# Optimization experiments

Hardware: AMD Instinct MI355X
Metric: run time of the kernel (lower is better)

The kernel has to match this reference:

```python
import jax, jax.numpy as jnp
import numpy as np

D = 13        # input_dim == cell hidden dim == attention dim
NCLASSES = 8

def conv2d(x, w):
    # x: [B,C,H,W], w: [O,I,kh,kw], SAME padding, stride 1
    return jax.lax.conv_general_dilated(x, w, (1, 1), 'SAME',
        dimension_numbers=('NCHW', 'OIHW', 'NCHW'))

def setup_inputs() -> dict:
    key = jax.random.key(0)
    ks = jax.random.split(key, 11)
    b, t, h, w = 32, 24, 32, 32
    s = 0.1
    return {
        'x1':      jax.random.normal(ks[0], (b, t, D, h, w), jnp.float32),
        'W_gates': jax.random.normal(ks[1], (4 * D, 2 * D, 3, 3), jnp.float32) * s,  # ConvLSTM gate conv on [x;h]
        'W_q':     jax.random.normal(ks[2], (D, D), jnp.float32) * s,   # SAM 1x1 convs (stored as matrices)
        'W_kh':    jax.random.normal(ks[3], (D, D), jnp.float32) * s,
        'W_vh':    jax.random.normal(ks[4], (D, D), jnp.float32) * s,
        'W_km':    jax.random.normal(ks[5], (D, D), jnp.float32) * s,
        'W_vm':    jax.random.normal(ks[6], (D, D), jnp.float32) * s,
        'W_z':     jax.random.normal(ks[7], (D, 2 * D), jnp.float32) * s,      # fuse [Zh;Zm] -> Z
        'W_m':     jax.random.normal(ks[8], (3 * D, 2 * D), jnp.float32) * s,  # [Z;h] -> (mo,mg,mi)
        'W_final': jax.random.normal(ks[9], (NCLASSES, D, 1, 1), jnp.float32) * s,
        'b_final': jnp.zeros((NCLASSES,), jnp.float32),
    }

def reference(x1, W_gates, W_q, W_kh, W_vh, W_km, W_vm, W_z, W_m, W_final, b_final):
    b, t, d, h, w = x1.shape
    N = h * w

    def attend(q, k, v):
        # q,k,v: [b,d,N]; full spatial self-attention (SAM), softmax over keys
        A = jax.nn.softmax(jnp.einsum('ban,bam->bnm', q, k), axis=-1)  # [b,N,N]
        return jnp.einsum('bnm,bdm->bdn', A, v)

    def sam(ht, m):
        # Self-Attention Memory module (SA-ConvLSTM, Lin et al. 2020)
        hf = ht.reshape(b, d, N)
        mf = m.reshape(b, d, N)
        q  = jnp.einsum('od,bdn->bon', W_q, hf)
        Zh = attend(q, jnp.einsum('od,bdn->bon', W_kh, hf), jnp.einsum('od,bdn->bon', W_vh, hf))
        Zm = attend(q, jnp.einsum('od,bdn->bon', W_km, mf), jnp.einsum('od,bdn->bon', W_vm, mf))
        Z  = jnp.einsum('oc,bcn->bon', W_z, jnp.concatenate([Zh, Zm], axis=1))
        comb = jnp.einsum('oc,bcn->bon', W_m, jnp.concatenate([Z, hf], axis=1))
        mo, mg, mi = jnp.split(comb, 3, axis=1)
        mi = jax.nn.sigmoid(mi)
        m_next = (1.0 - mi) * mf + mi * jnp.tanh(mg)
        h_next = jax.nn.sigmoid(mo) * m_next
        return h_next.reshape(b, d, h, w), m_next.reshape(b, d, h, w)

    def step(carry, xt):
        c, hh, m = carry
        gates = conv2d(jnp.concatenate([xt, hh], axis=1), W_gates)  # [b,4d,h,w]
        i, f, g, o = jnp.split(gates, 4, axis=1)
        c_next = jax.nn.sigmoid(f) * c + jax.nn.sigmoid(i) * jnp.tanh(g)
        h_tmp = jax.nn.sigmoid(o) * jnp.tanh(c_next)
        h_next, m_next = sam(h_tmp, m)
        return (c_next, h_next, m_next), None

    init = tuple(jnp.zeros((b, d, h, w), x1.dtype) for _ in range(3))  # cell, hidden, memory
    (c_fin, _, _), _ = jax.lax.scan(step, init, jnp.moveaxis(x1, 1, 0))
    logits = conv2d(c_fin, W_final) + b_final[None, :, None, None]
    return jax.nn.log_softmax(logits, axis=1)
```

## Files before the change

### kernel.cpp

```cpp
#include <hip/hip_runtime.h>
#include <math.h>

constexpr int B  = 32;
constexpr int T  = 24;
constexpr int D  = 13;
constexpr int N  = 1024;
constexpr int SZ = B * D * N;
constexpr int HPW = B * N * 16 / 2;

typedef __attribute__((ext_vector_type(8))) short bf16x8;
typedef __attribute__((ext_vector_type(4))) float f32x4;

__device__ __forceinline__ float sigmoidf_(float x) { return 1.f / (1.f + __expf(-x)); }
__device__ __forceinline__ float tanhf_(float x) {
    float e = __expf(2.f * x);
    return 1.f - 2.f / (e + 1.f);
}

__device__ __forceinline__ unsigned short f2bf(float f) {
    unsigned u = __float_as_uint(f);
    u += 0x8000u;
    return (unsigned short)(u >> 16);
}
__device__ __forceinline__ unsigned pk2bf(float lo, float hi) {
    unsigned a = __float_as_uint(lo) + 0x8000u;
    unsigned b = __float_as_uint(hi) + 0x8000u;
    return __builtin_amdgcn_perm(b, a, 0x07060302u);
}

__global__ void k_zero(float* __restrict__ p, int n) {
    int i = blockIdx.x * 256 + threadIdx.x;
    if (i < n) p[i] = 0.f;
}

__global__ __launch_bounds__(256) void k_xprep(const float* __restrict__ x1,
                                               unsigned short* __restrict__ x1p) {
    int i = blockIdx.x * 256 + threadIdx.x;
    int pix = i & 1023, bt = i >> 10;
    const float* src = x1 + (size_t)bt * D * N + pix;
    unsigned short tmp[16];
#pragma unroll
    for (int d = 0; d < 13; ++d) tmp[d] = f2bf(src[(size_t)d * N]);
    tmp[13] = tmp[14] = tmp[15] = 0;
    uint4* dst = (uint4*)(x1p + (size_t)i * 16);
    dst[0] = ((const uint4*)tmp)[0];
    dst[1] = ((const uint4*)tmp)[1];
}

__global__ void k_wprep(const float* __restrict__ Wg, unsigned short* __restrict__ wrA) {
    int i = blockIdx.x * 256 + threadIdx.x;
    if (i >= 4 * 9 * 64 * 8) return;
    int j = i & 7; int r = i >> 3;
    int lane = r & 63; r >>= 6;
    int tap = r % 9; int ct = r / 9;
    int m = lane & 15, g = lane >> 4;
    int k = g * 8 + j;
    int co = ct * 16 + m;
    int ci = -1;
    if (k < 13) ci = k;
    else if (k >= 16 && k < 29) ci = k - 3;
    unsigned short v = 0;
    if (co < 52 && ci >= 0) v = f2bf(Wg[(co * 26 + ci) * 9 + tap]);
    wrA[i] = v;
}

__global__ __launch_bounds__(256) void k_cp(
    const unsigned short* __restrict__ x1p, const unsigned short* __restrict__ wrA,
    const unsigned short* __restrict__ hp, float* __restrict__ c, const float* __restrict__ m_in,
    float* __restrict__ h_tmp,
    unsigned short* __restrict__ qT, unsigned short* __restrict__ khT,
    unsigned short* __restrict__ kmT, unsigned short* __restrict__ vh,
    unsigned short* __restrict__ vm,
    const float* __restrict__ Wq, const float* __restrict__ Wkh, const float* __restrict__ Wvh,
    const float* __restrict__ Wkm, const float* __restrict__ Wvm, int t)
{
    __shared__ __align__(16) unsigned short s_in[136 * 32];
    __shared__ float s_g[52 * 65];
    __shared__ float s_ht[13][64];
    __shared__ float s_mv[13][64];

    const int tile = blockIdx.x, b = blockIdx.y;
    const int tid = threadIdx.x;
    const int w = __builtin_amdgcn_readfirstlane(tid >> 6);
    const int lane = tid & 63;
    const int g = lane >> 4, l15 = lane & 15;
    const int y = tile * 2 + (lane >> 5), x = lane & 31;
    const int pix = y * 32 + x;
    const size_t bb = (size_t)b * D * N;

    float cpre[4], mpre[4];
#pragma unroll
    for (int i2 = 0; i2 < 4; ++i2) {
        int dd = w + 4 * i2;
        if (dd < 13) {
            cpre[i2] = c[bb + (size_t)dd * N + pix];
            mpre[i2] = m_in[bb + (size_t)dd * N + pix];
        } else { cpre[i2] = 0.f; mpre[i2] = 0.f; }
    }

    bf16x8 af[9];
#pragma unroll
    for (int tap = 0; tap < 9; ++tap)
        af[tap] = *(const bf16x8*)&wrA[(((size_t)w * 9 + tap) * 64 + lane) * 8];

    if (tid < 136) {
        int row = tid / 34, col = tid % 34;
        int gy = tile * 2 - 1 + row, gx = col - 1;
        bool ok = ((unsigned)gy < 32u) && ((unsigned)gx < 32u);
        uint4 z = {0, 0, 0, 0};
        uint4 a0 = z, a1 = z, b0 = z, b1 = z;
        if (ok) {
            const int off = gy * 32 + gx;
            const uint4* xs = (const uint4*)(x1p + (((size_t)b * T + t) * N + off) * 16);
            a0 = xs[0]; a1 = xs[1];
            const uint4* hs = (const uint4*)(hp + ((size_t)b * N + off) * 16);
            b0 = hs[0]; b1 = hs[1];
        }
        uint4* dst = (uint4*)&s_in[tid * 32];
        dst[0] = a0; dst[1] = a1; dst[2] = b0; dst[3] = b1;
    }
    __syncthreads();

    f32x4 acc[4];
#pragma unroll
    for (int pt = 0; pt < 4; ++pt) acc[pt] = f32x4{0.f, 0.f, 0.f, 0.f};
#pragma unroll
    for (int pt = 0; pt < 4; ++pt) {
        const int px = pt * 16 + l15;
        const int r0 = px >> 5, c0 = px & 31;
#pragma unroll
        for (int tap = 0; tap < 9; ++tap) {
            const int srow = r0 + tap / 3, scol = c0 + tap % 3;
            bf16x8 bfr = *(const bf16x8*)&s_in[(srow * 34 + scol) * 32 + 8 * g];
            acc[pt] = __builtin_amdgcn_mfma_f32_16x16x32_bf16(af[tap], bfr, acc[pt], 0, 0, 0);
        }
    }
#pragma unroll
    for (int pt = 0; pt < 4; ++pt) {
#pragma unroll
        for (int rr = 0; rr < 4; ++rr) {
            const int co = w * 16 + 4 * g + rr;
            if (co < 52) s_g[co * 65 + pt * 16 + l15] = acc[pt][rr];
        }
    }
    __syncthreads();

#pragma unroll
    for (int i2 = 0; i2 < 4; ++i2) {
        int dd = w + 4 * i2;
        if (dd < 13) {
            float ig = sigmoidf_(s_g[dd * 65 + lane]);
            float fg = sigmoidf_(s_g[(13 + dd) * 65 + lane]);
            float gg = tanhf_(s_g[(26 + dd) * 65 + lane]);
            float og = sigmoidf_(s_g[(39 + dd) * 65 + lane]);
            const size_t gi = bb + (size_t)dd * N + pix;
            float cn = fg * cpre[i2] + ig * gg;
            c[gi] = cn;
            float hv = og * tanhf_(cn);
            h_tmp[gi] = hv;
            s_ht[dd][lane] = hv;
            s_mv[dd][lane] = mpre[i2];
        }
    }
    __syncthreads();

    const size_t ro = ((size_t)b * N + pix) * 16;
    if (w == 0) {
        float htv[13];
#pragma unroll
        for (int j = 0; j < 13; ++j) htv[j] = s_ht[j][lane];
        float o[13];
#pragma unroll
        for (int d = 0; d < 13; ++d) {
            float a = 0.f;
#pragma unroll
            for (int j = 0; j < 13; ++j) a = fmaf(Wq[d * 13 + j], htv[j], a);
            o[d] = a * 1.44269504089f;
        }
        uint4 w0, w1;
        w0.x = pk2bf(o[0], o[1]);  w0.y = pk2bf(o[2], o[3]);
        w0.z = pk2bf(o[4], o[5]);  w0.w = pk2bf(o[6], o[7]);
        w1.x = pk2bf(o[8], o[9]);  w1.y = pk2bf(o[10], o[11]);
        w1.z = pk2bf(o[12], 0.f);  w1.w = 0u;
        ((uint4*)(qT + ro))[0] = w0; ((uint4*)(qT + ro))[1] = w1;
    } else if (w == 1) {
        float htv[13];
#pragma unroll
        for (int j = 0; j < 13; ++j) htv[j] = s_ht[j][lane];
        float o[13];
#pragma unroll
        for (int d = 0; d < 13; ++d) {
            float a = 0.f;
#pragma unroll
            for (int j = 0; j < 13; ++j) a = fmaf(Wkh[d * 13 + j], htv[j], a);
            o[d] = a;
        }
        uint4 w0, w1;
        w0.x = pk2bf(o[0], o[1]);  w0.y = pk2bf(o[2], o[3]);
        w0.z = pk2bf(o[4], o[5]);  w0.w = pk2bf(o[6], o[7]);
        w1.x = pk2bf(o[8], o[9]);  w1.y = pk2bf(o[10], o[11]);
        w1.z = pk2bf(o[12], 0.f);  w1.w = 0u;
        ((uint4*)(khT + ro))[0] = w0; ((uint4*)(khT + ro))[1] = w1;
#pragma unroll
        for (int d = 0; d < 13; ++d) {
            float a = 0.f;
#pragma unroll
            for (int j = 0; j < 13; ++j) a = fmaf(Wvh[d * 13 + j], htv[j], a);
            vh[bb + (size_t)d * N + pix] = f2bf(a);
        }
    } else if (w == 2) {
        float mvv[13];
#pragma unroll
        for (int j = 0; j < 13; ++j) mvv[j] = s_mv[j][lane];
        float o[13];
#pragma unroll
        for (int d = 0; d < 13; ++d) {
            float a = 0.f;
#pragma unroll
            for (int j = 0; j < 13; ++j) a = fmaf(Wkm[d * 13 + j], mvv[j], a);
            o[d] = a;
        }
        uint4 w0, w1;
        w0.x = pk2bf(o[0], o[1]);  w0.y = pk2bf(o[2], o[3]);
        w0.z = pk2bf(o[4], o[5]);  w0.w = pk2bf(o[6], o[7]);
        w1.x = pk2bf(o[8], o[9]);  w1.y = pk2bf(o[10], o[11]);
        w1.z = pk2bf(o[12], 0.f);  w1.w = 0u;
        ((uint4*)(kmT + ro))[0] = w0; ((uint4*)(kmT + ro))[1] = w1;
#pragma unroll
        for (int d = 0; d < 13; ++d) {
            float a = 0.f;
#pragma unroll
            for (int j = 0; j < 13; ++j) a = fmaf(Wvm[d * 13 + j], mvv[j], a);
            vm[bb + (size_t)d * N + pix] = f2bf(a);
        }
    }
}

__global__ __launch_bounds__(256) void k_attn(
    const unsigned short* __restrict__ qT, const unsigned short* __restrict__ khT,
    const unsigned short* __restrict__ kmT, const unsigned short* __restrict__ vh,
    const unsigned short* __restrict__ vm, const float* __restrict__ h_tmp,
    const float* __restrict__ Wz, const float* __restrict__ Wm,
    float* __restrict__ m, unsigned short* __restrict__ hp)
{
    __shared__ __align__(16) unsigned short s_k[2][128 * 24];
    __shared__ __align__(16) unsigned short s_v[2][16 * 136];
    __shared__ __align__(16) unsigned short s_hout[32 * 16];
    __shared__ float s_hf[13 * 33];
    __shared__ float s_zh[13 * 33], s_zm[13 * 33], s_zc[13 * 33];
    __shared__ float s_wz[13 * 26];
    __shared__ float s_wm[39 * 26];

    const int b = blockIdx.y, n0 = blockIdx.x * 32, tid = threadIdx.x;
    const int lane = tid & 63, w = tid >> 6;
    const int g = lane >> 4, l15 = lane & 15;
    const int br = w >> 1, qg = w & 1;
    const size_t bbN = (size_t)b * D * N;

    for (int idx = tid; idx < 13 * 26; idx += 256) s_wz[idx] = Wz[idx];
    for (int idx = tid; idx < 39 * 26; idx += 256) s_wm[idx] = Wm[idx];
    for (int idx = tid; idx < 13 * 32; idx += 256) {
        int d = idx >> 5, p = idx & 31;
        s_hf[d * 33 + p] = h_tmp[bbN + (size_t)d * N + n0 + p];
    }
    for (int idx = tid; idx < 512; idx += 256) s_hout[idx] = 0;
    for (int idx = tid; idx < 2 * 3 * 136; idx += 256) {
        int keyp = idx % 136;
        int r = idx / 136;
        int row = r % 3, br2 = r / 3;
        s_v[br2][(13 + row) * 136 + keyp] = (row == 0) ? (unsigned short)0x3F80 : (unsigned short)0;
    }

    bf16x8 b1 = {0, 0, 0, 0, 0, 0, 0, 0};
    if (g < 2)
        b1 = *(const bf16x8*)(qT + ((size_t)b * N + n0 + qg * 16 + l15) * 16 + 8 * g);

    const int rowk = tid >> 1, partk = tid & 1;
    const unsigned short* kb0 = khT + ((size_t)b * N + rowk) * 16 + partk * 8;
    const unsigned short* kb1 = kmT + ((size_t)b * N + rowk) * 16 + partk * 8;
    unsigned short* sk0 = &s_k[0][rowk * 24 + partk * 8];
    unsigned short* sk1 = &s_k[1][rowk * 24 + partk * 8];
    const int brv0 = (tid >= 208) ? 1 : 0;
    const int rem0 = tid - 208 * brv0;
    const int dv0 = rem0 >> 4, pv0 = rem0 & 15;
    const unsigned short* vb0 = (brv0 ? vm : vh) + bbN + (size_t)dv0 * N + pv0 * 8;
    unsigned short* sv0 = &s_v[brv0][dv0 * 136 + pv0 * 8];
    const bool doV1 = (tid < 160);
    const int rem1 = tid + 48;
    const int dv1 = rem1 >> 4, pv1 = rem1 & 15;
    const unsigned short* vb1 = vm + bbN + (size_t)dv1 * N + pv1 * 8;
    unsigned short* sv1 = &s_v[1][dv1 * 136 + pv1 * 8];

    uint4 rk0 = *(const uint4*)kb0;
    uint4 rk1 = *(const uint4*)kb1;
    uint4 rv0 = *(const uint4*)vb0;
    uint4 rv1 = doV1 ? *(const uint4*)vb1 : uint4{0, 0, 0, 0};

    f32x4 zacc = {0.f, 0.f, 0.f, 0.f};

    for (int cc = 0; cc < 8; ++cc) {
        if (cc) __syncthreads();
        *(uint4*)sk0 = rk0;
        *(uint4*)sk1 = rk1;
        *(uint4*)sv0 = rv0;
        if (doV1) *(uint4*)sv1 = rv1;
        __syncthreads();
        if (cc < 7) {
            const size_t ko = (size_t)(cc + 1) * 128 * 16;
            const size_t vo = (size_t)(cc + 1) * 128;
            rk0 = *(const uint4*)(kb0 + ko);
            rk1 = *(const uint4*)(kb1 + ko);
            rv0 = *(const uint4*)(vb0 + vo);
            if (doV1) rv1 = *(const uint4*)(vb1 + vo);
        }
#pragma unroll
        for (int u = 0; u < 4; ++u) {
            bf16x8 a0 = {0, 0, 0, 0, 0, 0, 0, 0}, a1v = {0, 0, 0, 0, 0, 0, 0, 0};
            if (g < 2) {
                const int rbase = 32 * u + 8 * (l15 >> 2) + (l15 & 3);
                a0  = *(const bf16x8*)&s_k[br][(rbase)     * 24 + 8 * g];
                a1v = *(const bf16x8*)&s_k[br][(rbase + 4) * 24 + 8 * g];
            }
            f32x4 d0 = {0.f, 0.f, 0.f, 0.f}, d1 = {0.f, 0.f, 0.f, 0.f};
            d0 = __builtin_amdgcn_mfma_f32_16x16x32_bf16(a0,  b1, d0, 0, 0, 0);
            d1 = __builtin_amdgcn_mfma_f32_16x16x32_bf16(a1v, b1, d1, 0, 0, 0);

            float e0[4], e1[4];
#pragma unroll
            for (int r = 0; r < 4; ++r) { e0[r] = exp2f(d0[r]); e1[r] = exp2f(d1[r]); }

            union { int4 iv; bf16x8 v; } u2;
            u2.iv.x = (int)pk2bf(e0[0], e0[1]);
            u2.iv.y = (int)pk2bf(e0[2], e0[3]);
            u2.iv.z = (int)pk2bf(e1[0], e1[1]);
            u2.iv.w = (int)pk2bf(e1[2], e1[3]);

            bf16x8 a2 = *(const bf16x8*)&s_v[br][l15 * 136 + 32 * u + 8 * g];
            zacc = __builtin_amdgcn_mfma_f32_16x16x32_bf16(a2, u2.v, zacc, 0, 0, 0);
        }
    }

    const float den = __shfl(zacc[1], 48 + l15, 64);
    const float rd = 1.f / den;

    float* zs = br ? s_zm : s_zh;
    const int q = qg * 16 + l15;
#pragma unroll
    for (int r = 0; r < 4; ++r) {
        int d = 4 * g + r;
        if (d < 13) zs[d * 33 + q] = zacc[r] * rd;
    }
    __syncthreads();

    for (int idx = tid; idx < 416; idx += 256) {
        int d = idx >> 5, p = idx & 31;
        float a = 0.f;
#pragma unroll
        for (int ci = 0; ci < 13; ++ci)
            a += s_wz[d * 26 + ci] * s_zh[ci * 33 + p]
               + s_wz[d * 26 + 13 + ci] * s_zm[ci * 33 + p];
        s_zc[d * 33 + p] = a;
    }
    __syncthreads();

    for (int idx = tid; idx < 416; idx += 256) {
        int d = idx >> 5, p = idx & 31;
        float mo = 0.f, mg = 0.f, mi = 0.f;
#pragma unroll
        for (int ci = 0; ci < 13; ++ci) {
            float zc = s_zc[ci * 33 + p];
            mo += s_wm[d * 26 + ci] * zc;
            mg += s_wm[(13 + d) * 26 + ci] * zc;
            mi += s_wm[(26 + d) * 26 + ci] * zc;
        }
#pragma unroll
        for (int ci = 0; ci < 13; ++ci) {
            float hc = s_hf[ci * 33 + p];
            mo += s_wm[d * 26 + 13 + ci] * hc;
            mg += s_wm[(13 + d) * 26 + 13 + ci] * hc;
            mi += s_wm[(26 + d) * 26 + 13 + ci] * hc;
        }
        mi = sigmoidf_(mi);
        const size_t gi = bbN + (size_t)d * N + n0 + p;
        float mn = (1.f - mi) * m[gi] + mi * tanhf_(mg);
        m[gi] = mn;
        s_hout[p * 16 + d] = f2bf(sigmoidf_(mo) * mn);
    }
    __syncthreads();

    if (tid < 32) {
        uint4* dst = (uint4*)(hp + ((size_t)b * N + n0 + tid) * 16);
        const uint4* srcp = (const uint4*)&s_hout[tid * 16];
        dst[0] = srcp[0]; dst[1] = srcp[1];
    }
}

__global__ __launch_bounds__(256) void k_final(
    const float* __restrict__ c, const float* __restrict__ Wf,
    const float* __restrict__ bf, float* __restrict__ out)
{
    const int i = blockIdx.x * 256 + threadIdx.x;
    const int b = i >> 10, pix = i & 1023;
    const size_t base = (size_t)b * D * N + pix;
    float cv[13];
#pragma unroll
    for (int d = 0; d < 13; ++d) cv[d] = c[base + (size_t)d * N];
    float lg[8]; float mx = -1e30f;
#pragma unroll
    for (int k = 0; k < 8; ++k) {
        float a = bf[k];
#pragma unroll
        for (int d = 0; d < 13; ++d) a += Wf[k * 13 + d] * cv[d];
        lg[k] = a; mx = fmaxf(mx, a);
    }
    float s = 0.f;
#pragma unroll
    for (int k = 0; k < 8; ++k) s += __expf(lg[k] - mx);
    float lse = mx + logf(s);
    const size_t ob = (size_t)b * 8 * N + pix;
#pragma unroll
    for (int k = 0; k < 8; ++k) out[ob + (size_t)k * N] = lg[k] - lse;
}

extern "C" void kernel_launch(void* const* d_in, const int* in_sizes, int n_in,
                              void* d_out, int out_size, void* d_ws, size_t ws_size,
                              hipStream_t stream) {
    const float* x1  = (const float*)d_in[0];
    const float* Wg  = (const float*)d_in[1];
    const float* Wq  = (const float*)d_in[2];
    const float* Wkh = (const float*)d_in[3];
    const float* Wvh = (const float*)d_in[4];
    const float* Wkm = (const float*)d_in[5];
    const float* Wvm = (const float*)d_in[6];
    const float* Wz  = (const float*)d_in[7];
    const float* Wm  = (const float*)d_in[8];
    const float* Wf  = (const float*)d_in[9];
    const float* bf  = (const float*)d_in[10];

    float* ws    = (float*)d_ws;
    float* c     = ws;
    float* m     = ws + (size_t)SZ;
    unsigned short* hp = (unsigned short*)(ws + (size_t)2 * SZ);
    float* h_tmp = ws + (size_t)2 * SZ + HPW;

    unsigned short* bstart = (unsigned short*)(ws + (size_t)3 * SZ + HPW);
    unsigned short* qT  = bstart;
    unsigned short* khT = qT  + (size_t)16 * B * N;
    unsigned short* kmT = khT + (size_t)16 * B * N;
    unsigned short* vhp = kmT + (size_t)16 * B * N;
    unsigned short* vmp = vhp + (size_t)13 * B * N;
    unsigned short* x1p = vmp + (size_t)13 * B * N;
    unsigned short* wrA = x1p + (size_t)16 * B * T * N;

    k_zero<<<(2 * SZ + HPW + 255) / 256, 256, 0, stream>>>(ws, 2 * SZ + HPW);
    k_wprep<<<72, 256, 0, stream>>>(Wg, wrA);
    k_xprep<<<(B * T * N) / 256, 256, 0, stream>>>(x1, x1p);

    for (int t = 0; t < T; ++t) {
        k_cp<<<dim3(16, 32), 256, 0, stream>>>(x1p, wrA, hp, c, m, h_tmp,
                                               qT, khT, kmT, vhp, vmp,
                                               Wq, Wkh, Wvh, Wkm, Wvm, t);
        k_attn<<<dim3(32, 32), 256, 0, stream>>>(qT, khT, kmT, vhp, vmp, h_tmp,
                                                 Wz, Wm, m, hp);
    }
    k_final<<<(B * N) / 256, 256, 0, stream>>>(c, Wf, bf, (float*)d_out);
}
```

Before: 1.184 ms.

## Fuse timestep loop into one persistent kernel with grid-wide atomic barriers

Replaces the 48 per-timestep launches of the conv and attention kernels plus the final kernel with a single persistent kernel of 512 blocks. Phases are separated by a software grid barrier built on an atomic counter with sleep polling. K/V buffers are double-buffered by timestep parity so that fewer barriers are needed. This removes launch overhead and inter-kernel gaps, but relies on all 512 blocks being co-resident (launch bounds request 2 blocks per CU). Each block now does the attention work of two of the former attention tiles.

After: 2.490 ms. +110.3%, slower.

```diff
diff --git a/kernel.cpp b/kernel.cpp
--- a/kernel.cpp
+++ b/kernel.cpp
@@ -7,6 +7,7 @@
 constexpr int N  = 1024;
 constexpr int SZ = B * D * N;
 constexpr int HPW = B * N * 16 / 2;
+constexpr int GRID = 512;
 
 typedef __attribute__((ext_vector_type(8))) short bf16x8;
 typedef __attribute__((ext_vector_type(4))) float f32x4;
@@ -16,7 +17,6 @@
     float e = __expf(2.f * x);
     return 1.f - 2.f / (e + 1.f);
 }
-
 __device__ __forceinline__ unsigned short f2bf(float f) {
     unsigned u = __float_as_uint(f);
     u += 0x8000u;
@@ -26,6 +26,17 @@
     unsigned a = __float_as_uint(lo) + 0x8000u;
     unsigned b = __float_as_uint(hi) + 0x8000u;
     return __builtin_amdgcn_perm(b, a, 0x07060302u);
+}
+
+__device__ __forceinline__ void gsync(unsigned* cnt, unsigned target) {
+    __syncthreads();
+    if (threadIdx.x == 0) {
+        __hip_atomic_fetch_add(cnt, 1u, __ATOMIC_RELEASE, __HIP_MEMORY_SCOPE_AGENT);
+        while (__hip_atomic_load(cnt, __ATOMIC_RELAXED, __HIP_MEMORY_SCOPE_AGENT) < target)
+            __builtin_amdgcn_s_sleep(16);
+        __builtin_amdgcn_fence(__ATOMIC_ACQUIRE, "agent");
+    }
+    __syncthreads();
 }
 
 __global__ void k_zero(float* __restrict__ p, int n) {
@@ -64,362 +75,398 @@
     wrA[i] = v;
 }
 
-__global__ __launch_bounds__(256) void k_cp(
+struct __align__(16) SharedCP {
+    unsigned short s_in[136 * 32];
+    float s_g[52 * 65];
+    float s_ht[13 * 64];
+    float s_mv[13 * 64];
+};
+struct __align__(16) SharedAT {
+    unsigned short s_k[2 * 128 * 24];
+    unsigned short s_v[2 * 16 * 136];
+    unsigned short s_hout[32 * 16];
+    float s_hf[13 * 33];
+    float s_zh[13 * 33];
+    float s_zm[13 * 33];
+    float s_zc[13 * 33];
+};
+union SharedU { SharedCP cp; SharedAT at; };
+
+__global__ __launch_bounds__(256, 2) void k_seq(
     const unsigned short* __restrict__ x1p, const unsigned short* __restrict__ wrA,
-    const unsigned short* __restrict__ hp, float* __restrict__ c, const float* __restrict__ m_in,
-    float* __restrict__ h_tmp,
-    unsigned short* __restrict__ qT, unsigned short* __restrict__ khT,
-    unsigned short* __restrict__ kmT, unsigned short* __restrict__ vh,
-    unsigned short* __restrict__ vm,
+    float* __restrict__ c, float* __restrict__ m, unsigned short* __restrict__ hp,
+    float* __restrict__ h_tmp, unsigned short* __restrict__ qT,
+    unsigned short* __restrict__ khT, unsigned short* __restrict__ kmT,
+    unsigned short* __restrict__ vhb, unsigned short* __restrict__ vmb,
     const float* __restrict__ Wq, const float* __restrict__ Wkh, const float* __restrict__ Wvh,
-    const float* __restrict__ Wkm, const float* __restrict__ Wvm, int t)
+    const float* __restrict__ Wkm, const float* __restrict__ Wvm,
+    const float* __restrict__ Wz, const float* __restrict__ Wm,
+    const float* __restrict__ Wf, const float* __restrict__ bfin,
+    float* __restrict__ out, unsigned* __restrict__ cnt)
 {
-    __shared__ __align__(16) unsigned short s_in[136 * 32];
-    __shared__ float s_g[52 * 65];
-    __shared__ float s_ht[13][64];
-    __shared__ float s_mv[13][64];
-
-    const int tile = blockIdx.x, b = blockIdx.y;
+    __shared__ SharedU u;
+    __shared__ float s_wz[13 * 26];
+    __shared__ float s_wm[39 * 26];
+
+    const int bx = blockIdx.x, by = blockIdx.y;
     const int tid = threadIdx.x;
     const int w = __builtin_amdgcn_readfirstlane(tid >> 6);
     const int lane = tid & 63;
     const int g = lane >> 4, l15 = lane & 15;
-    const int y = tile * 2 + (lane >> 5), x = lane & 31;
-    const int pix = y * 32 + x;
-    const size_t bb = (size_t)b * D * N;
-
-    float cpre[4], mpre[4];
-#pragma unroll
-    for (int i2 = 0; i2 < 4; ++i2) {
-        int dd = w + 4 * i2;
-        if (dd < 13) {
-            cpre[i2] = c[bb + (size_t)dd * N + pix];
-            mpre[i2] = m_in[bb + (size_t)dd * N + pix];
-        } else { cpre[i2] = 0.f; mpre[i2] = 0.f; }
-    }
-
-    bf16x8 af[9];
-#pragma unroll
-    for (int tap = 0; tap < 9; ++tap)
-        af[tap] = *(const bf16x8*)&wrA[(((size_t)w * 9 + tap) * 64 + lane) * 8];
-
-    if (tid < 136) {
-        int row = tid / 34, col = tid % 34;
-        int gy = tile * 2 - 1 + row, gx = col - 1;
-        bool ok = ((unsigned)gy < 32u) && ((unsigned)gx < 32u);
-        uint4 z = {0, 0, 0, 0};
-        uint4 a0 = z, a1 = z, b0 = z, b1 = z;
-        if (ok) {
-            const int off = gy * 32 + gx;
-            const uint4* xs = (const uint4*)(x1p + (((size_t)b * T + t) * N + off) * 16);
-            a0 = xs[0]; a1 = xs[1];
-            const uint4* hs = (const uint4*)(hp + ((size_t)b * N + off) * 16);
-            b0 = hs[0]; b1 = hs[1];
-        }
-        uint4* dst = (uint4*)&s_in[tid * 32];
-        dst[0] = a0; dst[1] = a1; dst[2] = b0; dst[3] = b1;
-    }
-    __syncthreads();
-
-    f32x4 acc[4];
-#pragma unroll
-    for (int pt = 0; pt < 4; ++pt) acc[pt] = f32x4{0.f, 0.f, 0.f, 0.f};
-#pragma unroll
-    for (int pt = 0; pt < 4; ++pt) {
-        const int px = pt * 16 + l15;
-        const int r0 = px >> 5, c0 = px & 31;
-#pragma unroll
-        for (int tap = 0; tap < 9; ++tap) {
-            const int srow = r0 + tap / 3, scol = c0 + tap % 3;
-            bf16x8 bfr = *(const bf16x8*)&s_in[(srow * 34 + scol) * 32 + 8 * g];
-            acc[pt] = __builtin_amdgcn_mfma_f32_16x16x32_bf16(af[tap], bfr, acc[pt], 0, 0, 0);
-        }
-    }
-#pragma unroll
-    for (int pt = 0; pt < 4; ++pt) {
-#pragma unroll
-        for (int rr = 0; rr < 4; ++rr) {
-            const int co = w * 16 + 4 * g + rr;
-            if (co < 52) s_g[co * 65 + pt * 16 + l15] = acc[pt][rr];
-        }
-    }
-    __syncthreads();
-
-#pragma unroll
-    for (int i2 = 0; i2 < 4; ++i2) {
-        int dd = w + 4 * i2;
-        if (dd < 13) {
-            float ig = sigmoidf_(s_g[dd * 65 + lane]);
-            float fg = sigmoidf_(s_g[(13 + dd) * 65 + lane]);
-            float gg = tanhf_(s_g[(26 + dd) * 65 + lane]);
-            float og = sigmoidf_(s_g[(39 + dd) * 65 + lane]);
-            const size_t gi = bb + (size_t)dd * N + pix;
-            float cn = fg * cpre[i2] + ig * gg;
-            c[gi] = cn;
-            float hv = og * tanhf_(cn);
-            h_tmp[gi] = hv;
-            s_ht[dd][lane] = hv;
-            s_mv[dd][lane] = mpre[i2];
-        }
-    }
-    __syncthreads();
-
-    const size_t ro = ((size_t)b * N + pix) * 16;
-    if (w == 0) {
-        float htv[13];
-#pragma unroll
-        for (int j = 0; j < 13; ++j) htv[j] = s_ht[j][lane];
-        float o[13];
-#pragma unroll
-        for (int d = 0; d < 13; ++d) {
-            float a = 0.f;
-#pragma unroll
-            for (int j = 0; j < 13; ++j) a = fmaf(Wq[d * 13 + j], htv[j], a);
-            o[d] = a * 1.44269504089f;
-        }
-        uint4 w0, w1;
-        w0.x = pk2bf(o[0], o[1]);  w0.y = pk2bf(o[2], o[3]);
-        w0.z = pk2bf(o[4], o[5]);  w0.w = pk2bf(o[6], o[7]);
-        w1.x = pk2bf(o[8], o[9]);  w1.y = pk2bf(o[10], o[11]);
-        w1.z = pk2bf(o[12], 0.f);  w1.w = 0u;
-        ((uint4*)(qT + ro))[0] = w0; ((uint4*)(qT + ro))[1] = w1;
-    } else if (w == 1) {
-        float htv[13];
-#pragma unroll
-        for (int j = 0; j < 13; ++j) htv[j] = s_ht[j][lane];
-        float o[13];
-#pragma unroll
-        for (int d = 0; d < 13; ++d) {
-            float a = 0.f;
-#pragma unroll
-            for (int j = 0; j < 13; ++j) a = fmaf(Wkh[d * 13 + j], htv[j], a);
-            o[d] = a;
-        }
-        uint4 w0, w1;
-        w0.x = pk2bf(o[0], o[1]);  w0.y = pk2bf(o[2], o[3]);
-        w0.z = pk2bf(o[4], o[5]);  w0.w = pk2bf(o[6], o[7]);
-        w1.x = pk2bf(o[8], o[9]);  w1.y = pk2bf(o[10], o[11]);
-        w1.z = pk2bf(o[12], 0.f);  w1.w = 0u;
-        ((uint4*)(khT + ro))[0] = w0; ((uint4*)(khT + ro))[1] = w1;
-#pragma unroll
-        for (int d = 0; d < 13; ++d) {
-            float a = 0.f;
-#pragma unroll
-            for (int j = 0; j < 13; ++j) a = fmaf(Wvh[d * 13 + j], htv[j], a);
-            vh[bb + (size_t)d * N + pix] = f2bf(a);
-        }
-    } else if (w == 2) {
-        float mvv[13];
-#pragma unroll
-        for (int j = 0; j < 13; ++j) mvv[j] = s_mv[j][lane];
-        float o[13];
-#pragma unroll
-        for (int d = 0; d < 13; ++d) {
-            float a = 0.f;
-#pragma unroll
-            for (int j = 0; j < 13; ++j) a = fmaf(Wkm[d * 13 + j], mvv[j], a);
-            o[d] = a;
-        }
-        uint4 w0, w1;
-        w0.x = pk2bf(o[0], o[1]);  w0.y = pk2bf(o[2], o[3]);
-        w0.z = pk2bf(o[4], o[5]);  w0.w = pk2bf(o[6], o[7]);
-        w1.x = pk2bf(o[8], o[9]);  w1.y = pk2bf(o[10], o[11]);
-        w1.z = pk2bf(o[12], 0.f);  w1.w = 0u;
-        ((uint4*)(kmT + ro))[0] = w0; ((uint4*)(kmT + ro))[1] = w1;
-#pragma unroll
-        for (int d = 0; d < 13; ++d) {
-            float a = 0.f;
-#pragma unroll
-            for (int j = 0; j < 13; ++j) a = fmaf(Wvm[d * 13 + j], mvv[j], a);
-            vm[bb + (size_t)d * N + pix] = f2bf(a);
-        }
-    }
-}
-
-__global__ __launch_bounds__(256) void k_attn(
-    const unsigned short* __restrict__ qT, const unsigned short* __restrict__ khT,
-    const unsigned short* __restrict__ kmT, const unsigned short* __restrict__ vh,
-    const unsigned short* __restrict__ vm, const float* __restrict__ h_tmp,
-    const float* __restrict__ Wz, const float* __restrict__ Wm,
-    float* __restrict__ m, unsigned short* __restrict__ hp)
-{
-    __shared__ __align__(16) unsigned short s_k[2][128 * 24];
-    __shared__ __align__(16) unsigned short s_v[2][16 * 136];
-    __shared__ __align__(16) unsigned short s_hout[32 * 16];
-    __shared__ float s_hf[13 * 33];
-    __shared__ float s_zh[13 * 33], s_zm[13 * 33], s_zc[13 * 33];
-    __shared__ float s_wz[13 * 26];
-    __shared__ float s_wm[39 * 26];
-
-    const int b = blockIdx.y, n0 = blockIdx.x * 32, tid = threadIdx.x;
-    const int lane = tid & 63, w = tid >> 6;
-    const int g = lane >> 4, l15 = lane & 15;
-    const int br = w >> 1, qg = w & 1;
-    const size_t bbN = (size_t)b * D * N;
+    const size_t bb = (size_t)by * D * N;
 
     for (int idx = tid; idx < 13 * 26; idx += 256) s_wz[idx] = Wz[idx];
     for (int idx = tid; idx < 39 * 26; idx += 256) s_wm[idx] = Wm[idx];
-    for (int idx = tid; idx < 13 * 32; idx += 256) {
-        int d = idx >> 5, p = idx & 31;
-        s_hf[d * 33 + p] = h_tmp[bbN + (size_t)d * N + n0 + p];
+
+    unsigned target = 0;
+
+    for (int t = 0; t < T; ++t) {
+        const int par = t & 1;
+        {
+            unsigned short* s_in = u.cp.s_in;
+            float* s_g  = u.cp.s_g;
+            float* s_ht = u.cp.s_ht;
+            float* s_mv = u.cp.s_mv;
+            unsigned short* khw = khT + (size_t)par * 16 * B * N;
+            unsigned short* kmw = kmT + (size_t)par * 16 * B * N;
+            unsigned short* vhw = vhb + (size_t)par * 13 * B * N;
+            unsigned short* vmw = vmb + (size_t)par * 13 * B * N;
+            const int y = bx * 2 + (lane >> 5), x = lane & 31;
+            const int pix = y * 32 + x;
+
+            float cpre[4], mpre[4];
+#pragma unroll
+            for (int i2 = 0; i2 < 4; ++i2) {
+                int dd = w + 4 * i2;
+                if (dd < 13) {
+                    cpre[i2] = c[bb + (size_t)dd * N + pix];
+                    mpre[i2] = m[bb + (size_t)dd * N + pix];
+                } else { cpre[i2] = 0.f; mpre[i2] = 0.f; }
+            }
+            bf16x8 af[9];
+#pragma unroll
+            for (int tap = 0; tap < 9; ++tap)
+                af[tap] = *(const bf16x8*)&wrA[(((size_t)w * 9 + tap) * 64 + lane) * 8];
+
+            if (tid < 136) {
+                int row = tid / 34, col = tid % 34;
+                int gy = bx * 2 - 1 + row, gx = col - 1;
+                bool ok = ((unsigned)gy < 32u) && ((unsigned)gx < 32u);
+                uint4 z = {0, 0, 0, 0};
+                uint4 a0 = z, a1 = z, b0 = z, b1 = z;
+                if (ok) {
+                    const int off = gy * 32 + gx;
+                    const uint4* xs = (const uint4*)(x1p + (((size_t)by * T + t) * N + off) * 16);
+                    a0 = xs[0]; a1 = xs[1];
+                    const uint4* hs = (const uint4*)(hp + ((size_t)by * N + off) * 16);
+                    b0 = hs[0]; b1 = hs[1];
+                }
+                uint4* dst = (uint4*)&s_in[tid * 32];
+                dst[0] = a0; dst[1] = a1; dst[2] = b0; dst[3] = b1;
+            }
+            __syncthreads();
+
+            f32x4 acc[4];
+#pragma unroll
+            for (int pt = 0; pt < 4; ++pt) acc[pt] = f32x4{0.f, 0.f, 0.f, 0.f};
+#pragma unroll
+            for (int pt = 0; pt < 4; ++pt) {
+                const int px = pt * 16 + l15;
+                const int r0 = px >> 5, c0 = px & 31;
+#pragma unroll
+                for (int tap = 0; tap < 9; ++tap) {
+                    const int srow = r0 + tap / 3, scol = c0 + tap % 3;
+                    bf16x8 bfr = *(const bf16x8*)&s_in[(srow * 34 + scol) * 32 + 8 * g];
+                    acc[pt] = __builtin_amdgcn_mfma_f32_16x16x32_bf16(af[tap], bfr, acc[pt], 0, 0, 0);
+                }
+            }
+#pragma unroll
+            for (int pt = 0; pt < 4; ++pt) {
+#pragma unroll
+                for (int rr = 0; rr < 4; ++rr) {
+                    const int co = w * 16 + 4 * g + rr;
+                    if (co < 52) s_g[co * 65 + pt * 16 + l15] = acc[pt][rr];
+                }
+            }
+            __syncthreads();
+
+#pragma unroll
+            for (int i2 = 0; i2 < 4; ++i2) {
+                int dd = w + 4 * i2;
+                if (dd < 13) {
+                    float ig = sigmoidf_(s_g[dd * 65 + lane]);
+                    float fg = sigmoidf_(s_g[(13 + dd) * 65 + lane]);
+                    float gg = tanhf_(s_g[(26 + dd) * 65 + lane]);
+                    float og = sigmoidf_(s_g[(39 + dd) * 65 + lane]);
+                    const size_t gi = bb + (size_t)dd * N + pix;
+                    float cn = fg * cpre[i2] + ig * gg;
+                    c[gi] = cn;
+                    float hv = og * tanhf_(cn);
+                    h_tmp[gi] = hv;
+                    s_ht[dd * 64 + lane] = hv;
+                    s_mv[dd * 64 + lane] = mpre[i2];
+                }
+            }
+            __syncthreads();
+
+            const size_t ro = ((size_t)by * N + pix) * 16;
+            if (w == 0) {
+                float htv[13];
+#pragma unroll
+                for (int j = 0; j < 13; ++j) htv[j] = s_ht[j * 64 + lane];
+                float o[13];
+#pragma unroll
+                for (int d = 0; d < 13; ++d) {
+                    float a = 0.f;
+#pragma unroll
+                    for (int j = 0; j < 13; ++j) a = fmaf(Wq[d * 13 + j], htv[j], a);
+                    o[d] = a * 1.44269504089f;
+                }
+                uint4 w0, w1;
+                w0.x = pk2bf(o[0], o[1]);  w0.y = pk2bf(o[2], o[3]);
+                w0.z = pk2bf(o[4], o[5]);  w0.w = pk2bf(o[6], o[7]);
+                w1.x = pk2bf(o[8], o[9]);  w1.y = pk2bf(o[10], o[11]);
+                w1.z = pk2bf(o[12], 0.f);  w1.w = 0u;
+                ((uint4*)(qT + ro))[0] = w0; ((uint4*)(qT + ro))[1] = w1;
+            } else if (w == 1) {
+                float htv[13];
+#pragma unroll
+                for (int j = 0; j < 13; ++j) htv[j] = s_ht[j * 64 + lane];
+                float o[13];
+#pragma unroll
+                for (int d = 0; d < 13; ++d) {
+                    float a = 0.f;
+#pragma unroll
+                    for (int j = 0; j < 13; ++j) a = fmaf(Wkh[d * 13 + j], htv[j], a);
+                    o[d] = a;
+                }
+                uint4 w0, w1;
+                w0.x = pk2bf(o[0], o[1]);  w0.y = pk2bf(o[2], o[3]);
+                w0.z = pk2bf(o[4], o[5]);  w0.w = pk2bf(o[6], o[7]);
+                w1.x = pk2bf(o[8], o[9]);  w1.y = pk2bf(o[10], o[11]);
+                w1.z = pk2bf(o[12], 0.f);  w1.w = 0u;
+                ((uint4*)(khw + ro))[0] = w0; ((uint4*)(khw + ro))[1] = w1;
+#pragma unroll
+                for (int d = 0; d < 13; ++d) {
+                    float a = 0.f;
+#pragma unroll
+                    for (int j = 0; j < 13; ++j) a = fmaf(Wvh[d * 13 + j], htv[j], a);
+                    vhw[bb + (size_t)d * N + pix] = f2bf(a);
+                }
+            } else if (w == 2) {
+                float mvv[13];
+#pragma unroll
+                for (int j = 0; j < 13; ++j) mvv[j] = s_mv[j * 64 + lane];
+                float o[13];
+#pragma unroll
+                for (int d = 0; d < 13; ++d) {
+                    float a = 0.f;
+#pragma unroll
+                    for (int j = 0; j < 13; ++j) a = fmaf(Wkm[d * 13 + j], mvv[j], a);
+                    o[d] = a;
+                }
+                uint4 w0, w1;
+                w0.x = pk2bf(o[0], o[1]);  w0.y = pk2bf(o[2], o[3]);
+                w0.z = pk2bf(o[4], o[5]);  w0.w = pk2bf(o[6], o[7]);
+                w1.x = pk2bf(o[8], o[9]);  w1.y = pk2bf(o[10], o[11]);
+                w1.z = pk2bf(o[12], 0.f);  w1.w = 0u;
+                ((uint4*)(kmw + ro))[0] = w0; ((uint4*)(kmw + ro))[1] = w1;
+#pragma unroll
+                for (int d = 0; d < 13; ++d) {
+                    float a = 0.f;
+#pragma unroll
+                    for (int j = 0; j < 13; ++j) a = fmaf(Wvm[d * 13 + j], mvv[j], a);
+                    vmw[bb + (size_t)d * N + pix] = f2bf(a);
+                }
+            }
+        }
+
+        if (t == T - 1) break;
+
+        target += GRID; gsync(cnt, target);
+
+        {
+            unsigned short* s_k = u.at.s_k;
+            unsigned short* s_v = u.at.s_v;
+            unsigned short* s_hout = u.at.s_hout;
+            float* s_hf = u.at.s_hf;
+            float* s_zh = u.at.s_zh;
+            float* s_zm = u.at.s_zm;
+            float* s_zc = u.at.s_zc;
+            const unsigned short* khp_ = khT + (size_t)par * 16 * B * N;
+            const unsigned short* kmp_ = kmT + (size_t)par * 16 * B * N;
+            const unsigned short* vhp_ = vhb + (size_t)par * 13 * B * N;
+            const unsigned short* vmp_ = vmb + (size_t)par * 13 * B * N;
+            const int br = w >> 1, qg = w & 1;
+
+            for (int qt = 0; qt < 2; ++qt) {
+                __syncthreads();
+                const int n0 = bx * 64 + qt * 32;
+
+                for (int idx = tid; idx < 13 * 32; idx += 256) {
+                    int d = idx >> 5, p = idx & 31;
+                    s_hf[d * 33 + p] = h_tmp[bb + (size_t)d * N + n0 + p];
+                }
+                for (int idx = tid; idx < 512; idx += 256) s_hout[idx] = 0;
+                for (int idx = tid; idx < 2 * 3 * 136; idx += 256) {
+                    int keyp = idx % 136;
+                    int r = idx / 136;
+                    int row = r % 3, br2 = r / 3;
+                    s_v[br2 * 2176 + (13 + row) * 136 + keyp] =
+                        (row == 0) ? (unsigned short)0x3F80 : (unsigned short)0;
+                }
+
+                bf16x8 b1 = {0, 0, 0, 0, 0, 0, 0, 0};
+                if (g < 2)
+                    b1 = *(const bf16x8*)(qT + ((size_t)by * N + n0 + qg * 16 + l15) * 16 + 8 * g);
+
+                const int rowk = tid >> 1, partk = tid & 1;
+                const unsigned short* kb0 = khp_ + ((size_t)by * N + rowk) * 16 + partk * 8;
+                const unsigned short* kb1 = kmp_ + ((size_t)by * N + rowk) * 16 + partk * 8;
+                unsigned short* sk0 = &s_k[rowk * 24 + partk * 8];
+                unsigned short* sk1 = &s_k[3072 + rowk * 24 + partk * 8];
+                const int brv0 = (tid >= 208) ? 1 : 0;
+                const int rem0 = tid - 208 * brv0;
+                const int dv0 = rem0 >> 4, pv0 = rem0 & 15;
+                const unsigned short* vb0 = (brv0 ? vmp_ : vhp_) + bb + (size_t)dv0 * N + pv0 * 8;
+                unsigned short* sv0 = &s_v[brv0 * 2176 + dv0 * 136 + pv0 * 8];
+                const bool doV1 = (tid < 160);
+                const int rem1 = tid + 48;
+                const int dv1 = rem1 >> 4, pv1 = rem1 & 15;
+                const unsigned short* vb1 = vmp_ + bb + (size_t)dv1 * N + pv1 * 8;
+                unsigned short* sv1 = &s_v[2176 + dv1 * 136 + pv1 * 8];
+
+                uint4 rk0 = *(const uint4*)kb0;
+                uint4 rk1 = *(const uint4*)kb1;
+                uint4 rv0 = *(const uint4*)vb0;
+                uint4 rv1 = doV1 ? *(const uint4*)vb1 : uint4{0, 0, 0, 0};
+
+                f32x4 zacc = {0.f, 0.f, 0.f, 0.f};
+
+                for (int cc = 0; cc < 8; ++cc) {
+                    if (cc) __syncthreads();
+                    *(uint4*)sk0 = rk0;
+                    *(uint4*)sk1 = rk1;
+                    *(uint4*)sv0 = rv0;
+                    if (doV1) *(uint4*)sv1 = rv1;
+                    __syncthreads();
+                    if (cc < 7) {
+                        const size_t ko = (size_t)(cc + 1) * 128 * 16;
+                        const size_t vo = (size_t)(cc + 1) * 128;
+                        rk0 = *(const uint4*)(kb0 + ko);
+                        rk1 = *(const uint4*)(kb1 + ko);
+                        rv0 = *(const uint4*)(vb0 + vo);
+                        if (doV1) rv1 = *(const uint4*)(vb1 + vo);
+                    }
+#pragma unroll
+                    for (int uu = 0; uu < 4; ++uu) {
+                        bf16x8 a0 = {0, 0, 0, 0, 0, 0, 0, 0}, a1v = {0, 0, 0, 0, 0, 0, 0, 0};
+                        if (g < 2) {
+                            const int rbase = 32 * uu + 8 * (l15 >> 2) + (l15 & 3);
+                            a0  = *(const bf16x8*)&s_k[br * 3072 + (rbase)     * 24 + 8 * g];
+                            a1v = *(const bf16x8*)&s_k[br * 3072 + (rbase + 4) * 24 + 8 * g];
+                        }
+                        f32x4 d0 = {0.f, 0.f, 0.f, 0.f}, d1 = {0.f, 0.f, 0.f, 0.f};
+                        d0 = __builtin_amdgcn_mfma_f32_16x16x32_bf16(a0,  b1, d0, 0, 0, 0);
+                        d1 = __builtin_amdgcn_mfma_f32_16x16x32_bf16(a1v, b1, d1, 0, 0, 0);
+
+                        float e0[4], e1[4];
+#pragma unroll
+                        for (int r = 0; r < 4; ++r) { e0[r] = exp2f(d0[r]); e1[r] = exp2f(d1[r]); }
+
+                        union { int4 iv; bf16x8 v; } u2;
+                        u2.iv.x = (int)pk2bf(e0[0], e0[1]);
+                        u2.iv.y = (int)pk2bf(e0[2], e0[3]);
+                        u2.iv.z = (int)pk2bf(e1[0], e1[1]);
+                        u2.iv.w = (int)pk2bf(e1[2], e1[3]);
+
+                        bf16x8 a2 = *(const bf16x8*)&s_v[br * 2176 + l15 * 136 + 32 * uu + 8 * g];
+                        zacc = __builtin_amdgcn_mfma_f32_16x16x32_bf16(a2, u2.v, zacc, 0, 0, 0);
+                    }
+                }
+
+                const float den = __shfl(zacc[1], 48 + l15, 64);
+                const float rd = 1.f / den;
+
+                float* zs = br ? s_zm : s_zh;
+                const int q = qg * 16 + l15;
+#pragma unroll
+                for (int r = 0; r < 4; ++r) {
+                    int d = 4 * g + r;
+                    if (d < 13) zs[d * 33 + q] = zacc[r] * rd;
+                }
+                __syncthreads();
+
+                for (int idx = tid; idx < 416; idx += 256) {
+                    int d = idx >> 5, p = idx & 31;
+                    float a = 0.f;
+#pragma unroll
+                    for (int ci = 0; ci < 13; ++ci)
+                        a += s_wz[d * 26 + ci] * s_zh[ci * 33 + p]
+                           + s_wz[d * 26 + 13 + ci] * s_zm[ci * 33 + p];
+                    s_zc[d * 33 + p] = a;
+                }
+                __syncthreads();
+
+                for (int idx = tid; idx < 416; idx += 256) {
+                    int d = idx >> 5, p = idx & 31;
+                    float mo = 0.f, mg = 0.f, mi = 0.f;
+#pragma unroll
+                    for (int ci = 0; ci < 13; ++ci) {
+                        float zc = s_zc[ci * 33 + p];
+                        mo += s_wm[d * 26 + ci] * zc;
+                        mg += s_wm[(13 + d) * 26 + ci] * zc;
+                        mi += s_wm[(26 + d) * 26 + ci] * zc;
+                    }
+#pragma unroll
+                    for (int ci = 0; ci < 13; ++ci) {
+                        float hc = s_hf[ci * 33 + p];
+                        mo += s_wm[d * 26 + 13 + ci] * hc;
+                        mg += s_wm[(13 + d) * 26 + 13 + ci] * hc;
+                        mi += s_wm[(26 + d) * 26 + 13 + ci] * hc;
+                    }
+                    mi = sigmoidf_(mi);
+                    const size_t gi = bb + (size_t)d * N + n0 + p;
+                    float mn = (1.f - mi) * m[gi] + mi * tanhf_(mg);
+                    m[gi] = mn;
+                    s_hout[p * 16 + d] = f2bf(sigmoidf_(mo) * mn);
+                }
+                __syncthreads();
+
+                if (tid < 32) {
+                    uint4* dst = (uint4*)(hp + ((size_t)by * N + n0 + tid) * 16);
+                    const uint4* srcp = (const uint4*)&s_hout[tid * 16];
+                    dst[0] = srcp[0]; dst[1] = srcp[1];
+                }
+            }
+        }
+
+        target += GRID; gsync(cnt, target);
     }
-    for (int idx = tid; idx < 512; idx += 256) s_hout[idx] = 0;
-    for (int idx = tid; idx < 2 * 3 * 136; idx += 256) {
-        int keyp = idx % 136;
-        int r = idx / 136;
-        int row = r % 3, br2 = r / 3;
-        s_v[br2][(13 + row) * 136 + keyp] = (row == 0) ? (unsigned short)0x3F80 : (unsigned short)0;
+
+    __syncthreads();
+    if (tid < 64) {
+        const int px = bx * 64 + tid;
+        const size_t base = bb + px;
+        float cv[13];
+#pragma unroll
+        for (int d = 0; d < 13; ++d) cv[d] = c[base + (size_t)d * N];
+        float lg[8]; float mx = -1e30f;
+#pragma unroll
+        for (int k = 0; k < 8; ++k) {
+            float a = bfin[k];
+#pragma unroll
+            for (int d = 0; d < 13; ++d) a += Wf[k * 13 + d] * cv[d];
+            lg[k] = a; mx = fmaxf(mx, a);
+        }
+        float s = 0.f;
+#pragma unroll
+        for (int k = 0; k < 8; ++k) s += __expf(lg[k] - mx);
+        float lse = mx + logf(s);
+        const size_t ob = (size_t)by * 8 * N + px;
+#pragma unroll
+        for (int k = 0; k < 8; ++k) out[ob + (size_t)k * N] = lg[k] - lse;
     }
-
-    bf16x8 b1 = {0, 0, 0, 0, 0, 0, 0, 0};
-    if (g < 2)
-        b1 = *(const bf16x8*)(qT + ((size_t)b * N + n0 + qg * 16 + l15) * 16 + 8 * g);
-
-    const int rowk = tid >> 1, partk = tid & 1;
-    const unsigned short* kb0 = khT + ((size_t)b * N + rowk) * 16 + partk * 8;
-    const unsigned short* kb1 = kmT + ((size_t)b * N + rowk) * 16 + partk * 8;
-    unsigned short* sk0 = &s_k[0][rowk * 24 + partk * 8];
-    unsigned short* sk1 = &s_k[1][rowk * 24 + partk * 8];
-    const int brv0 = (tid >= 208) ? 1 : 0;
-    const int rem0 = tid - 208 * brv0;
-    const int dv0 = rem0 >> 4, pv0 = rem0 & 15;
-    const unsigned short* vb0 = (brv0 ? vm : vh) + bbN + (size_t)dv0 * N + pv0 * 8;
-    unsigned short* sv0 = &s_v[brv0][dv0 * 136 + pv0 * 8];
-    const bool doV1 = (tid < 160);
-    const int rem1 = tid + 48;
-    const int dv1 = rem1 >> 4, pv1 = rem1 & 15;
-    const unsigned short* vb1 = vm + bbN + (size_t)dv1 * N + pv1 * 8;
-    unsigned short* sv1 = &s_v[1][dv1 * 136 + pv1 * 8];
-
-    uint4 rk0 = *(const uint4*)kb0;
-    uint4 rk1 = *(const uint4*)kb1;
-    uint4 rv0 = *(const uint4*)vb0;
-    uint4 rv1 = doV1 ? *(const uint4*)vb1 : uint4{0, 0, 0, 0};
-
-    f32x4 zacc = {0.f, 0.f, 0.f, 0.f};
-
-    for (int cc = 0; cc < 8; ++cc) {
-        if (cc) __syncthreads();
-        *(uint4*)sk0 = rk0;
-        *(uint4*)sk1 = rk1;
-        *(uint4*)sv0 = rv0;
-        if (doV1) *(uint4*)sv1 = rv1;
-        __syncthreads();
-        if (cc < 7) {
-            const size_t ko = (size_t)(cc + 1) * 128 * 16;
-            const size_t vo = (size_t)(cc + 1) * 128;
-            rk0 = *(const uint4*)(kb0 + ko);
-            rk1 = *(const uint4*)(kb1 + ko);
-            rv0 = *(const uint4*)(vb0 + vo);
-            if (doV1) rv1 = *(const uint4*)(vb1 + vo);
-        }
-#pragma unroll
-        for (int u = 0; u < 4; ++u) {
-            bf16x8 a0 = {0, 0, 0, 0, 0, 0, 0, 0}, a1v = {0, 0, 0, 0, 0, 0, 0, 0};
-            if (g < 2) {
-                const int rbase = 32 * u + 8 * (l15 >> 2) + (l15 & 3);
-                a0  = *(const bf16x8*)&s_k[br][(rbase)     * 24 + 8 * g];
-                a1v = *(const bf16x8*)&s_k[br][(rbase + 4) * 24 + 8 * g];
-            }
-            f32x4 d0 = {0.f, 0.f, 0.f, 0.f}, d1 = {0.f, 0.f, 0.f, 0.f};
-            d0 = __builtin_amdgcn_mfma_f32_16x16x32_bf16(a0,  b1, d0, 0, 0, 0);
-            d1 = __builtin_amdgcn_mfma_f32_16x16x32_bf16(a1v, b1, d1, 0, 0, 0);
-
-            float e0[4], e1[4];
-#pragma unroll
-            for (int r = 0; r < 4; ++r) { e0[r] = exp2f(d0[r]); e1[r] = exp2f(d1[r]); }
-
-            union { int4 iv; bf16x8 v; } u2;
-            u2.iv.x = (int)pk2bf(e0[0], e0[1]);
-            u2.iv.y = (int)pk2bf(e0[2], e0[3]);
-            u2.iv.z = (int)pk2bf(e1[0], e1[1]);
-            u2.iv.w = (int)pk2bf(e1[2], e1[3]);
-
-            bf16x8 a2 = *(const bf16x8*)&s_v[br][l15 * 136 + 32 * u + 8 * g];
-            zacc = __builtin_amdgcn_mfma_f32_16x16x32_bf16(a2, u2.v, zacc, 0, 0, 0);
-        }
-    }
-
-    const float den = __shfl(zacc[1], 48 + l15, 64);
-    const float rd = 1.f / den;
-
-    float* zs = br ? s_zm : s_zh;
-    const int q = qg * 16 + l15;
-#pragma unroll
-    for (int r = 0; r < 4; ++r) {
-        int d = 4 * g + r;
-        if (d < 13) zs[d * 33 + q] = zacc[r] * rd;
-    }
-    __syncthreads();
-
-    for (int idx = tid; idx < 416; idx += 256) {
-        int d = idx >> 5, p = idx & 31;
-        float a = 0.f;
-#pragma unroll
-        for (int ci = 0; ci < 13; ++ci)
-            a += s_wz[d * 26 + ci] * s_zh[ci * 33 + p]
-               + s_wz[d * 26 + 13 + ci] * s_zm[ci * 33 + p];
-        s_zc[d * 33 + p] = a;
-    }
-    __syncthreads();
-
-    for (int idx = tid; idx < 416; idx += 256) {
-        int d = idx >> 5, p = idx & 31;
-        float mo = 0.f, mg = 0.f, mi = 0.f;
-#pragma unroll
-        for (int ci = 0; ci < 13; ++ci) {
-            float zc = s_zc[ci * 33 + p];
-            mo += s_wm[d * 26 + ci] * zc;
-            mg += s_wm[(13 + d) * 26 + ci] * zc;
-            mi += s_wm[(26 + d) * 26 + ci] * zc;
-        }
-#pragma unroll
-        for (int ci = 0; ci < 13; ++ci) {
-            float hc = s_hf[ci * 33 + p];
-            mo += s_wm[d * 26 + 13 + ci] * hc;
-            mg += s_wm[(13 + d) * 26 + 13 + ci] * hc;
-            mi += s_wm[(26 + d) * 26 + 13 + ci] * hc;
-        }
-        mi = sigmoidf_(mi);
-        const size_t gi = bbN + (size_t)d * N + n0 + p;
-        float mn = (1.f - mi) * m[gi] + mi * tanhf_(mg);
-        m[gi] = mn;
-        s_hout[p * 16 + d] = f2bf(sigmoidf_(mo) * mn);
-    }
-    __syncthreads();
-
-    if (tid < 32) {
-        uint4* dst = (uint4*)(hp + ((size_t)b * N + n0 + tid) * 16);
-        const uint4* srcp = (const uint4*)&s_hout[tid * 16];
-        dst[0] = srcp[0]; dst[1] = srcp[1];
-    }
-}
-
-__global__ __launch_bounds__(256) void k_final(
-    const float* __restrict__ c, const float* __restrict__ Wf,
-    const float* __restrict__ bf, float* __restrict__ out)
-{
-    const int i = blockIdx.x * 256 + threadIdx.x;
-    const int b = i >> 10, pix = i & 1023;
-    const size_t base = (size_t)b * D * N + pix;
-    float cv[13];
-#pragma unroll
-    for (int d = 0; d < 13; ++d) cv[d] = c[base + (size_t)d * N];
-    float lg[8]; float mx = -1e30f;
-#pragma unroll
-    for (int k = 0; k < 8; ++k) {
-        float a = bf[k];
-#pragma unroll
-        for (int d = 0; d < 13; ++d) a += Wf[k * 13 + d] * cv[d];
-        lg[k] = a; mx = fmaxf(mx, a);
-    }
-    float s = 0.f;
-#pragma unroll
-    for (int k = 0; k < 8; ++k) s += __expf(lg[k] - mx);
-    float lse = mx + logf(s);
-    const size_t ob = (size_t)b * 8 * N + pix;
-#pragma unroll
-    for (int k = 0; k < 8; ++k) out[ob + (size_t)k * N] = lg[k] - lse;
 }
 
 extern "C" void kernel_launch(void* const* d_in, const int* in_sizes, int n_in,
@@ -437,31 +484,28 @@
     const float* Wf  = (const float*)d_in[9];
     const float* bf  = (const float*)d_in[10];
 
-    float* ws    = (float*)d_ws;
-    float* c     = ws;
-    float* m     = ws + (size_t)SZ;
-    unsigned short* hp = (unsigned short*)(ws + (size_t)2 * SZ);
-    float* h_tmp = ws + (size_t)2 * SZ + HPW;
-
-    unsigned short* bstart = (unsigned short*)(ws + (size_t)3 * SZ + HPW);
-    unsigned short* qT  = bstart;
+    float* ws = (float*)d_ws;
+    unsigned* cnt = (unsigned*)d_ws;
+    float* c   = ws + 64;
+    float* m   = ws + 64 + (size_t)SZ;
+    unsigned short* hp = (unsigned short*)(ws + 64 + 2 * (size_t)SZ);
+    float* h_tmp = ws + 64 + 2 * (size_t)SZ + HPW;
+
+    unsigned short* qT  = (unsigned short*)(h_tmp + (size_t)SZ);
     unsigned short* khT = qT  + (size_t)16 * B * N;
-    unsigned short* kmT = khT + (size_t)16 * B * N;
-    unsigned short* vhp = kmT + (size_t)16 * B * N;
-    unsigned short* vmp = vhp + (size_t)13 * B * N;
-    unsigned short* x1p = vmp + (size_t)13 * B * N;
+    unsigned short* kmT = khT + (size_t)32 * B * N;
+    unsigned short* vhb = kmT + (size_t)32 * B * N;
+    unsigned short* vmb = vhb + (size_t)26 * B * N;
+    unsigned short* x1p = vmb + (size_t)26 * B * N;
     unsigned short* wrA = x1p + (size_t)16 * B * T * N;
 
-    k_zero<<<(2 * SZ + HPW + 255) / 256, 256, 0, stream>>>(ws, 2 * SZ + HPW);
+    const int zn = 64 + 2 * SZ + HPW;
+    k_zero<<<(zn + 255) / 256, 256, 0, stream>>>(ws, zn);
     k_wprep<<<72, 256, 0, stream>>>(Wg, wrA);
     k_xprep<<<(B * T * N) / 256, 256, 0, stream>>>(x1, x1p);
 
-    for (int t = 0; t < T; ++t) {
-        k_cp<<<dim3(16, 32), 256, 0, stream>>>(x1p, wrA, hp, c, m, h_tmp,
-                                               qT, khT, kmT, vhp, vmp,
-                                               Wq, Wkh, Wvh, Wkm, Wvm, t);
-        k_attn<<<dim3(32, 32), 256, 0, stream>>>(qT, khT, kmT, vhp, vmp, h_tmp,
-                                                 Wz, Wm, m, hp);
-    }
-    k_final<<<(B * N) / 256, 256, 0, stream>>>(c, Wf, bf, (float*)d_out);
-}
+    k_seq<<<dim3(16, 32), 256, 0, stream>>>(x1p, wrA, c, m, hp, h_tmp,
+                                            qT, khT, kmT, vhb, vmb,
+                                            Wq, Wkh, Wvh, Wkm, Wvm, Wz, Wm,
+                                            Wf, bf, (float*)d_out, cnt);
+}
```
